# Kernel tuning notes

Hardware: AMD Instinct MI355X
Metric: run time of the kernel (lower is better)

## Reference

```python
import jax, jax.numpy as jnp
import numpy as np

B, T, V, E, H, U = 32, 64, 32000, 300, 512, 512


def setup_inputs() -> dict:
    key = jax.random.key(0)
    ks = jax.random.split(key, 14)
    s = 0.05  # weight scale to keep gates in a sane range
    return {
        "trg_seq": jax.random.randint(ks[0], (B, T), 0, V, dtype=jnp.int32),
        "init_h": jax.random.normal(ks[1], (1, B, U), jnp.float32),
        "init_c": jax.random.normal(ks[2], (1, B, U), jnp.float32),
        "embedding": jax.random.normal(ks[3], (V, E), jnp.float32) * s,
        "Wh": jax.random.normal(ks[4], (H, U), jnp.float32) * s,
        "bh": jax.random.normal(ks[5], (H,), jnp.float32) * s,
        "Wc": jax.random.normal(ks[6], (H, U), jnp.float32) * s,
        "bc": jax.random.normal(ks[7], (H,), jnp.float32) * s,
        "W_ih": jax.random.normal(ks[8], (4 * H, E), jnp.float32) * s,
        "W_hh": jax.random.normal(ks[9], (4 * H, H), jnp.float32) * s,
        "b_ih": jax.random.normal(ks[10], (4 * H,), jnp.float32) * s,
        "b_hh": jax.random.normal(ks[11], (4 * H,), jnp.float32) * s,
        "W_logit": jax.random.normal(ks[12], (V, H), jnp.float32) * s,
        "b_logit": jax.random.normal(ks[13], (V,), jnp.float32) * s,
    }


def reference(trg_seq, init_h, init_c, embedding, Wh, bh, Wc, bc,
              W_ih, W_hh, b_ih, b_hh, W_logit, b_logit):
    # form_init: linear transform of encoder states -> LSTM initial h/c
    h0 = init_h[0] @ Wh.T + bh  # [B, H]
    c0 = init_c[0] @ Wc.T + bc  # [B, H]

    emb = embedding[trg_seq]                       # [B, T, E]
    x_gates = jnp.einsum('bte,ge->btg', emb, W_ih) + b_ih + b_hh  # [B, T, 4H]

    def step(carry, xg_t):
        h, c = carry
        gates = xg_t + h @ W_hh.T                  # [B, 4H]
        i, f, g, o = jnp.split(gates, 4, axis=-1)  # torch gate order i,f,g,o
        i, f, o = jax.nn.sigmoid(i), jax.nn.sigmoid(f), jax.nn.sigmoid(o)
        g = jnp.tanh(g)
        c = f * c + i * g
        h = o * jnp.tanh(c)
        return (h, c), h

    _, hs = jax.lax.scan(step, (h0, c0), x_gates.transpose(1, 0, 2))  # hs: [T, B, H]
    logits = jnp.tanh(hs) @ W_logit.T + b_logit    # [T, B, V]
    return logits.transpose(1, 0, 2)               # [B, T, V]
```

## Files before the change

### kernel.cpp

```cpp
#include <hip/hip_runtime.h>
#include <hip/hip_cooperative_groups.h>

typedef unsigned short u16;
typedef __attribute__((ext_vector_type(8))) unsigned short us8;
typedef __attribute__((ext_vector_type(8))) __bf16 bf16x8;
typedef __attribute__((ext_vector_type(4))) float f32x4;

#define B_ 32
#define T_ 64
#define V_ 32000
#define E_ 300
#define H_ 512
#define G4_ 2048
#define NBLK_ 32
#define NG_   224
#define NT_TILES 250
#define NM_TILES 16

__device__ __forceinline__ u16 f2b(float f){
  unsigned int x = __builtin_bit_cast(unsigned int, f);
  unsigned int r = (x + 0x7FFFu + ((x >> 16) & 1u)) >> 16;
  return (u16)r;
}
__device__ __forceinline__ float sigm(float x){ return 1.0f/(1.0f+expf(-x)); }

__device__ __forceinline__ void gload16(const u16* g, u16* l){
  __builtin_amdgcn_global_load_lds(
      (const __attribute__((address_space(1))) void*)g,
      (__attribute__((address_space(3))) void*)l, 16, 0, 0);
}

__global__ __launch_bounds__(256) void k_init(
    const float* __restrict__ init_h, const float* __restrict__ init_c,
    const float* __restrict__ Wh, const float* __restrict__ bh,
    const float* __restrict__ Wc, const float* __restrict__ bc,
    float* __restrict__ h0out, float* __restrict__ c0out,
    unsigned int* __restrict__ flag)
{
  if (blockIdx.x == 0){ flag[threadIdx.x] = 0u; flag[threadIdx.x + 256] = 0u; }
  int idx = blockIdx.x*blockDim.x + threadIdx.x;
  int sel = idx >> 14;
  int r = idx & 16383;
  int b = r >> 9, j = r & 511;
  const float* x = (sel ? init_c : init_h) + b*H_;
  const float* w = (sel ? Wc : Wh) + (size_t)j*H_;
  const float* bias = sel ? bc : bh;
  float acc = 0.f;
  for (int k = 0; k < H_; k += 8){
    f32x4 x0 = *(const f32x4*)(x + k), x1 = *(const f32x4*)(x + k + 4);
    f32x4 w0 = *(const f32x4*)(w + k), w1 = *(const f32x4*)(w + k + 4);
    acc += x0[0]*w0[0] + x0[1]*w0[1] + x0[2]*w0[2] + x0[3]*w0[3];
    acc += x1[0]*w1[0] + x1[1]*w1[1] + x1[2]*w1[2] + x1[3]*w1[3];
  }
  acc += bias[j];
  (sel ? c0out : h0out)[b*H_ + j] = acc;
}

__global__ __launch_bounds__(256) void k_cvt(
    const float* __restrict__ W, u16* __restrict__ W16)
{
  size_t i = ((size_t)blockIdx.x*256 + threadIdx.x)*8;
  f32x4 a = *(const f32x4*)(W + i);
  f32x4 b = *(const f32x4*)(W + i + 4);
  us8 u;
  u[0]=f2b(a[0]); u[1]=f2b(a[1]); u[2]=f2b(a[2]); u[3]=f2b(a[3]);
  u[4]=f2b(b[0]); u[5]=f2b(b[1]); u[6]=f2b(b[2]); u[7]=f2b(b[3]);
  *(us8*)(W16 + i) = u;
}

__global__ __launch_bounds__(256) void k_xgates(
    const float* __restrict__ emb, const float* __restrict__ Wih,
    const int* __restrict__ trg, const float* __restrict__ bih,
    const float* __restrict__ bhh, float* __restrict__ xg)
{
  __shared__ u16 As[128][40];
  __shared__ u16 Bs[128][40];
  const int bn0 = blockIdx.x*128, bm0 = blockIdx.y*128;
  const int tid = threadIdx.x;
  const int w = tid>>6, lane = tid&63;
  const int wr = w>>1, wc = w&1, lr = lane&15, lk = lane>>4;
  const int srow = tid>>1, half = tid&1;
  const int R = bm0 + srow;
  const int tt = R>>5, bb = R&31;
  const int token = trg[bb*T_ + tt];
  const float* arow = emb + (size_t)token*E_;
  const float* brow = Wih + (size_t)(bn0+srow)*E_;
  f32x4 acc[4][4] = {};
  for (int k0 = 0; k0 < E_; k0 += 32){
    int cbase = k0 + half*16;
    if (k0 + 32 <= E_){
      f32x4 a0=*(const f32x4*)(arow+cbase),    a1=*(const f32x4*)(arow+cbase+4);
      f32x4 a2=*(const f32x4*)(arow+cbase+8),  a3=*(const f32x4*)(arow+cbase+12);
      f32x4 b0=*(const f32x4*)(brow+cbase),    b1=*(const f32x4*)(brow+cbase+4);
      f32x4 b2=*(const f32x4*)(brow+cbase+8),  b3=*(const f32x4*)(brow+cbase+12);
      us8 ua, ub;
      ua[0]=f2b(a0[0]); ua[1]=f2b(a0[1]); ua[2]=f2b(a0[2]); ua[3]=f2b(a0[3]);
      ua[4]=f2b(a1[0]); ua[5]=f2b(a1[1]); ua[6]=f2b(a1[2]); ua[7]=f2b(a1[3]);
      ub[0]=f2b(a2[0]); ub[1]=f2b(a2[1]); ub[2]=f2b(a2[2]); ub[3]=f2b(a2[3]);
      ub[4]=f2b(a3[0]); ub[5]=f2b(a3[1]); ub[6]=f2b(a3[2]); ub[7]=f2b(a3[3]);
      *(us8*)&As[srow][half*16]   = ua;
      *(us8*)&As[srow][half*16+8] = ub;
      us8 va, vb;
      va[0]=f2b(b0[0]); va[1]=f2b(b0[1]); va[2]=f2b(b0[2]); va[3]=f2b(b0[3]);
      va[4]=f2b(b1[0]); va[5]=f2b(b1[1]); va[6]=f2b(b1[2]); va[7]=f2b(b1[3]);
      vb[0]=f2b(b2[0]); vb[1]=f2b(b2[1]); vb[2]=f2b(b2[2]); vb[3]=f2b(b2[3]);
      vb[4]=f2b(b3[0]); vb[5]=f2b(b3[1]); vb[6]=f2b(b3[2]); vb[7]=f2b(b3[3]);
      *(us8*)&Bs[srow][half*16]   = va;
      *(us8*)&Bs[srow][half*16+8] = vb;
    } else {
      for (int i = 0; i < 16; i++){
        int c = cbase + i;
        As[srow][half*16+i] = (c < E_) ? f2b(arow[c]) : (u16)0;
        Bs[srow][half*16+i] = (c < E_) ? f2b(brow[c]) : (u16)0;
      }
    }
    __syncthreads();
    bf16x8 af[4], bfr[4];
    #pragma unroll
    for (int m = 0; m < 4; m++) af[m] = *(const bf16x8*)&As[wr*64 + m*16 + lr][lk*8];
    #pragma unroll
    for (int n = 0; n < 4; n++) bfr[n] = *(const bf16x8*)&Bs[wc*64 + n*16 + lr][lk*8];
    #pragma unroll
    for (int m = 0; m < 4; m++)
      #pragma unroll
      for (int n = 0; n < 4; n++)
        acc[m][n] = __builtin_amdgcn_mfma_f32_16x16x32_bf16(af[m], bfr[n], acc[m][n], 0, 0, 0);
    __syncthreads();
  }
  #pragma unroll
  for (int n = 0; n < 4; n++){
    int col = bn0 + wc*64 + n*16 + lr;
    float bv = bih[col] + bhh[col];
    #pragma unroll
    for (int m = 0; m < 4; m++){
      #pragma unroll
      for (int i = 0; i < 4; i++){
        int row = bm0 + wr*64 + m*16 + lk*4 + i;
        xg[(size_t)row*G4_ + col] = acc[m][n][i] + bv;
      }
    }
  }
}

__global__ __launch_bounds__(512, 4) void k_mega(
    const float* __restrict__ Whh, const float* __restrict__ xg,
    const float* __restrict__ h0, const float* __restrict__ c0,
    u16* __restrict__ h_g, u16* __restrict__ A_buf,
    unsigned int* __restrict__ flag,
    const u16* __restrict__ W16, const float* __restrict__ bias,
    float* __restrict__ out)
{
  __shared__ __align__(16) char smem[41472];
  const int tid = threadIdx.x;

  if (blockIdx.x < NBLK_){
    u16 (*hl)[520] = (u16(*)[520])smem;
    float (*gb)[32][16] = (float(*)[32][16])(smem + 33280);
    const int bj = blockIdx.x;
    const int wv = tid >> 6, lane = tid & 63;
    const int g = wv >> 1, m = wv & 1;
    const int lr = lane & 15, lk = lane >> 4;

    bf16x8 bw[16];
    {
      const float* wsrc = Whh + (size_t)(g*H_ + bj*16 + lr)*H_;
      #pragma unroll
      for (int ks = 0; ks < 16; ks++){
        f32x4 w0 = *(const f32x4*)(wsrc + ks*32 + lk*8);
        f32x4 w1 = *(const f32x4*)(wsrc + ks*32 + lk*8 + 4);
        us8 u;
        u[0]=f2b(w0[0]); u[1]=f2b(w0[1]); u[2]=f2b(w0[2]); u[3]=f2b(w0[3]);
        u[4]=f2b(w1[0]); u[5]=f2b(w1[1]); u[6]=f2b(w1[2]); u[7]=f2b(w1[3]);
        bw[ks] = __builtin_bit_cast(bf16x8, u);
      }
    }
    const int ub = tid >> 4, uj = tid & 15;
    float c_reg = c0[ub*H_ + bj*16 + uj];

    {
      int r = tid >> 4, seg = tid & 15;
      const float* src = h0 + r*H_ + seg*32;
      #pragma unroll
      for (int q = 0; q < 4; q++){
        f32x4 v0 = *(const f32x4*)(src + q*8);
        f32x4 v1 = *(const f32x4*)(src + q*8 + 4);
        us8 u;
        u[0]=f2b(v0[0]); u[1]=f2b(v0[1]); u[2]=f2b(v0[2]); u[3]=f2b(v0[3]);
        u[4]=f2b(v1[0]); u[5]=f2b(v1[1]); u[6]=f2b(v1[2]); u[7]=f2b(v1[3]);
        *(us8*)&hl[r][seg*32 + q*8] = u;
      }
    }
    __syncthreads();

    for (int t = 0; t < T_; t++){
      const float* xr = xg + (size_t)t*(B_*G4_) + ub*G4_ + bj*16 + uj;
      float x0 = xr[0*H_], x1 = xr[1*H_], x2 = xr[2*H_], x3 = xr[3*H_];

      f32x4 acc = {0.f, 0.f, 0.f, 0.f};
      #pragma unroll
      for (int ks = 0; ks < 16; ks++){
        bf16x8 a = *(const bf16x8*)&hl[m*16 + lr][ks*32 + lk*8];
        acc = __builtin_amdgcn_mfma_f32_16x16x32_bf16(a, bw[ks], acc, 0, 0, 0);
      }
      #pragma unroll
      for (int i = 0; i < 4; i++)
        gb[g][m*16 + lk*4 + i][lr] = acc[i];
      __syncthreads();

      float gi = sigm(gb[0][ub][uj] + x0);
      float gf = sigm(gb[1][ub][uj] + x1);
      float gg = tanhf(gb[2][ub][uj] + x2);
      float go = sigm(gb[3][ub][uj] + x3);
      c_reg = gf*c_reg + gi*gg;
      float h = go * tanhf(c_reg);
      int p = (t+1) & 1;
      h_g[p*(B_*H_) + bj*(B_*16) + tid] = f2b(h);

      __syncthreads();
      if (t < T_-1 && tid == 0)
        __hip_atomic_store(&flag[bj*16], (unsigned)(t+1),
                           __ATOMIC_RELEASE, __HIP_MEMORY_SCOPE_AGENT);

      A_buf[(size_t)t*(B_*H_) + ub*H_ + bj*16 + uj] = f2b(tanhf(h));
      if (t == T_-1) break;

      if (tid < 64){
        unsigned want = (unsigned)(t+1), guard = 0;
        while (__hip_atomic_load(&flag[(tid&31)*16], __ATOMIC_ACQUIRE,
                                 __HIP_MEMORY_SCOPE_AGENT) < want
               && guard < (1u<<18)) { __builtin_amdgcn_s_sleep(1); ++guard; }
      }
      __syncthreads();

      {
        int r = tid >> 4, seg = tid & 15;
        const u16* hb = h_g + p*(B_*H_);
        const u16* p0 = hb + (seg*2)  *(B_*16) + r*16;
        const u16* p1 = hb + (seg*2+1)*(B_*16) + r*16;
        us8 v0 = *(const us8*)(p0);
        us8 v1 = *(const us8*)(p0 + 8);
        us8 v2 = *(const us8*)(p1);
        us8 v3 = *(const us8*)(p1 + 8);
        *(us8*)&hl[r][seg*32]      = v0;
        *(us8*)&hl[r][seg*32 + 8]  = v1;
        *(us8*)&hl[r][seg*32 + 16] = v2;
        *(us8*)&hl[r][seg*32 + 24] = v3;
      }
      __syncthreads();
    }
    __syncthreads();
    if (tid == 0)
      __hip_atomic_store(&flag[bj*16], 65u,
                         __ATOMIC_RELEASE, __HIP_MEMORY_SCOPE_AGENT);
  } else {
    u16* As = (u16*)smem;
    u16* Bs = (u16*)(smem + 8192);
    const int w = tid>>6, lane = tid&63;
    const int wr = w & 1, wc = w >> 1;
    const int lr = lane&15, lk = lane>>4;
    const int srow = w*16 + (lane>>2);
    const int cb   = ((lane&3)*16) ^ (((srow>>1)&3)<<4);
    u16* adst = &As[(w*16)*32];
    u16* bdst = &Bs[(w*16)*32];
    const int nt0 = (int)blockIdx.x - NBLK_;

    for (int mt = 0; mt < NM_TILES; mt++){
      const unsigned want = (mt < 15) ? (unsigned)(4*mt + 5) : 65u;
      if (tid < 64){
        unsigned guard = 0;
        for (;;){
          unsigned v = __hip_atomic_load(&flag[(tid&31)*16], __ATOMIC_RELAXED,
                                         __HIP_MEMORY_SCOPE_AGENT);
          if (__all(v >= want) || guard > (1u<<20)) break;
          __builtin_amdgcn_s_sleep(16); ++guard;
        }
        __builtin_amdgcn_fence(__ATOMIC_ACQUIRE, "agent");
      }
      __syncthreads();

      const int bm0 = mt*128;
      for (int nt = nt0; nt < NT_TILES; nt += NG_){
        const int bn0 = nt*128;
        const u16* aptr = A_buf + (size_t)(bm0+srow)*H_ + (cb>>1);
        const u16* bptr = W16   + (size_t)(bn0+srow)*H_ + (cb>>1);
        f32x4 acc[4][2] = {};
        for (int k0 = 0; k0 < H_; k0 += 32){
          gload16(aptr + k0, adst);
          gload16(bptr + k0, bdst);
          __syncthreads();
          bf16x8 af[4], bfr[2];
          #pragma unroll
          for (int m = 0; m < 4; m++){
            int row = wr*64 + m*16 + lr;
            af[m] = *(const bf16x8*)((const char*)As + row*64 + ((lk*16) ^ (((row>>1)&3)<<4)));
          }
          #pragma unroll
          for (int n = 0; n < 2; n++){
            int row = wc*32 + n*16 + lr;
            bfr[n] = *(const bf16x8*)((const char*)Bs + row*64 + ((lk*16) ^ (((row>>1)&3)<<4)));
          }
          #pragma unroll
          for (int m = 0; m < 4; m++)
            #pragma unroll
            for (int n = 0; n < 2; n++)
              acc[m][n] = __builtin_amdgcn_mfma_f32_16x16x32_bf16(af[m], bfr[n], acc[m][n], 0, 0, 0);
          __syncthreads();
        }
        #pragma unroll
        for (int n = 0; n < 2; n++){
          int col = bn0 + wc*32 + n*16 + lr;
          float bv = bias[col];
          #pragma unroll
          for (int m = 0; m < 4; m++){
            #pragma unroll
            for (int i = 0; i < 4; i++){
              int row = bm0 + wr*64 + m*16 + lk*4 + i;
              int t = row>>5, b = row&31;
              __builtin_nontemporal_store(acc[m][n][i] + bv,
                  &out[(size_t)b*((size_t)T_*V_) + (size_t)t*V_ + col]);
            }
          }
        }
      }
    }
  }
}

__global__ __launch_bounds__(512) void k_scan(
    const float* __restrict__ Whh, const float* __restrict__ xg,
    const float* __restrict__ h0, const float* __restrict__ c0,
    u16* __restrict__ h_g, u16* __restrict__ A_buf,
    unsigned int* __restrict__ flag)
{
  __shared__ u16 hl[32][520];
  __shared__ float gb[4][32][16];
  const int bj = blockIdx.x;
  const int tid = threadIdx.x;
  const int wv = tid >> 6, lane = tid & 63;
  const int g = wv >> 1, m = wv & 1;
  const int lr = lane & 15, lk = lane >> 4;
  bf16x8 bw[16];
  {
    const float* wsrc = Whh + (size_t)(g*H_ + bj*16 + lr)*H_;
    #pragma unroll
    for (int ks = 0; ks < 16; ks++){
      f32x4 w0 = *(const f32x4*)(wsrc + ks*32 + lk*8);
      f32x4 w1 = *(const f32x4*)(wsrc + ks*32 + lk*8 + 4);
      us8 u;
      u[0]=f2b(w0[0]); u[1]=f2b(w0[1]); u[2]=f2b(w0[2]); u[3]=f2b(w0[3]);
      u[4]=f2b(w1[0]); u[5]=f2b(w1[1]); u[6]=f2b(w1[2]); u[7]=f2b(w1[3]);
      bw[ks] = __builtin_bit_cast(bf16x8, u);
    }
  }
  const int ub = tid >> 4, uj = tid & 15;
  float c_reg = c0[ub*H_ + bj*16 + uj];
  {
    int r = tid >> 4, seg = tid & 15;
    const float* src = h0 + r*H_ + seg*32;
    #pragma unroll
    for (int q = 0; q < 4; q++){
      f32x4 v0 = *(const f32x4*)(src + q*8);
      f32x4 v1 = *(const f32x4*)(src + q*8 + 4);
      us8 u;
      u[0]=f2b(v0[0]); u[1]=f2b(v0[1]); u[2]=f2b(v0[2]); u[3]=f2b(v0[3]);
      u[4]=f2b(v1[0]); u[5]=f2b(v1[1]); u[6]=f2b(v1[2]); u[7]=f2b(v1[3]);
      *(us8*)&hl[r][seg*32 + q*8] = u;
    }
  }
  __syncthreads();
  for (int t = 0; t < T_; t++){
    const float* xr = xg + (size_t)t*(B_*G4_) + ub*G4_ + bj*16 + uj;
    float x0 = xr[0*H_], x1 = xr[1*H_], x2 = xr[2*H_], x3 = xr[3*H_];
    f32x4 acc = {0.f, 0.f, 0.f, 0.f};
    #pragma unroll
    for (int ks = 0; ks < 16; ks++){
      bf16x8 a = *(const bf16x8*)&hl[m*16 + lr][ks*32 + lk*8];
      acc = __builtin_amdgcn_mfma_f32_16x16x32_bf16(a, bw[ks], acc, 0, 0, 0);
    }
    #pragma unroll
    for (int i = 0; i < 4; i++)
      gb[g][m*16 + lk*4 + i][lr] = acc[i];
    __syncthreads();
    float gi = sigm(gb[0][ub][uj] + x0);
    float gf = sigm(gb[1][ub][uj] + x1);
    float gg = tanhf(gb[2][ub][uj] + x2);
    float go = sigm(gb[3][ub][uj] + x3);
    c_reg = gf*c_reg + gi*gg;
    float h = go * tanhf(c_reg);
    int p = (t+1) & 1;
    h_g[p*(B_*H_) + bj*(B_*16) + tid] = f2b(h);
    __syncthreads();
    if (t < T_-1 && tid == 0)
      __hip_atomic_store(&flag[bj*16], (unsigned)(t+1),
                         __ATOMIC_RELEASE, __HIP_MEMORY_SCOPE_AGENT);
    A_buf[(size_t)t*(B_*H_) + ub*H_ + bj*16 + uj] = f2b(tanhf(h));
    if (t == T_-1) break;
    if (tid < 64){
      unsigned want = (unsigned)(t+1), guard = 0;
      while (__hip_atomic_load(&flag[(tid&31)*16], __ATOMIC_ACQUIRE,
                               __HIP_MEMORY_SCOPE_AGENT) < want
             && guard < (1u<<18)) { __builtin_amdgcn_s_sleep(1); ++guard; }
    }
    __syncthreads();
    {
      int r = tid >> 4, seg = tid & 15;
      const u16* hb = h_g + p*(B_*H_);
      const u16* p0 = hb + (seg*2)  *(B_*16) + r*16;
      const u16* p1 = hb + (seg*2+1)*(B_*16) + r*16;
      us8 v0 = *(const us8*)(p0);
      us8 v1 = *(const us8*)(p0 + 8);
      us8 v2 = *(const us8*)(p1);
      us8 v3 = *(const us8*)(p1 + 8);
      *(us8*)&hl[r][seg*32]      = v0;
      *(us8*)&hl[r][seg*32 + 8]  = v1;
      *(us8*)&hl[r][seg*32 + 16] = v2;
      *(us8*)&hl[r][seg*32 + 24] = v3;
    }
    __syncthreads();
  }
}

__global__ __launch_bounds__(256) void k_logits16(
    const u16* __restrict__ A, const u16* __restrict__ W16,
    const float* __restrict__ bias, float* __restrict__ out)
{
  __shared__ u16 As[128*32];
  __shared__ u16 Bs[128*32];
  int bid = blockIdx.y*16 + blockIdx.x;
  int nbid = (bid & 7)*500 + (bid >> 3);
  const int bm0 = (nbid & 15)*128;
  const int bn0 = (nbid >> 4)*128;
  const int tid = threadIdx.x;
  const int w = tid>>6, lane = tid&63;
  const int wr = w>>1, wc = w&1, lr = lane&15, lk = lane>>4;
  const int srow = w*32 + (lane>>2);
  const int cb   = ((lane&3)*16) ^ (((srow>>1)&3)<<4);
  const u16* aptr = A   + (size_t)(bm0+srow)*H_ + (cb>>1);
  const u16* bptr = W16 + (size_t)(bn0+srow)*H_ + (cb>>1);
  u16* adst0 = &As[(w*32)*32];
  u16* adst1 = &As[(w*32+16)*32];
  u16* bdst0 = &Bs[(w*32)*32];
  u16* bdst1 = &Bs[(w*32+16)*32];
  f32x4 acc[4][4] = {};
  for (int k0 = 0; k0 < H_; k0 += 32){
    gload16(aptr + k0,          adst0);
    gload16(aptr + k0 + 16*H_,  adst1);
    gload16(bptr + k0,          bdst0);
    gload16(bptr + k0 + 16*H_,  bdst1);
    __syncthreads();
    bf16x8 af[4], bfr[4];
    #pragma unroll
    for (int m = 0; m < 4; m++){
      int row = wr*64 + m*16 + lr;
      af[m] = *(const bf16x8*)((const char*)As + row*64 + ((lk*16) ^ (((row>>1)&3)<<4)));
    }
    #pragma unroll
    for (int n = 0; n < 4; n++){
      int row = wc*64 + n*16 + lr;
      bfr[n] = *(const bf16x8*)((const char*)Bs + row*64 + ((lk*16) ^ (((row>>1)&3)<<4)));
    }
    #pragma unroll
    for (int m = 0; m < 4; m++)
      #pragma unroll
      for (int n = 0; n < 4; n++)
        acc[m][n] = __builtin_amdgcn_mfma_f32_16x16x32_bf16(af[m], bfr[n], acc[m][n], 0, 0, 0);
    __syncthreads();
  }
  #pragma unroll
  for (int n = 0; n < 4; n++){
    int col = bn0 + wc*64 + n*16 + lr;
    float bv = bias[col];
    #pragma unroll
    for (int m = 0; m < 4; m++){
      #pragma unroll
      for (int i = 0; i < 4; i++){
        int row = bm0 + wr*64 + m*16 + lk*4 + i;
        int t = row>>5, b = row&31;
        __builtin_nontemporal_store(acc[m][n][i] + bv,
            &out[(size_t)b*((size_t)T_*V_) + (size_t)t*V_ + col]);
      }
    }
  }
}

__global__ __launch_bounds__(256) void k_logits(
    const u16* __restrict__ A, const float* __restrict__ W,
    const float* __restrict__ bias, float* __restrict__ out)
{
  __shared__ u16 As[128][40];
  __shared__ u16 Bs[128][40];
  const int bm0 = blockIdx.x*128, bn0 = blockIdx.y*128;
  const int tid = threadIdx.x;
  const int w = tid>>6, lane = tid&63;
  const int wr = w>>1, wc = w&1, lr = lane&15, lk = lane>>4;
  const int srow = tid>>1, half = tid&1;
  const u16*   arow = A + (size_t)(bm0+srow)*H_;
  const float* brow = W + (size_t)(bn0+srow)*H_;
  f32x4 acc[4][4] = {};
  for (int k0 = 0; k0 < H_; k0 += 32){
    us8 a0 = *(const us8*)(arow + k0 + half*16);
    us8 a1 = *(const us8*)(arow + k0 + half*16 + 8);
    f32x4 b0 = *(const f32x4*)(brow + k0 + half*16);
    f32x4 b1 = *(const f32x4*)(brow + k0 + half*16 + 4);
    f32x4 b2 = *(const f32x4*)(brow + k0 + half*16 + 8);
    f32x4 b3 = *(const f32x4*)(brow + k0 + half*16 + 12);
    *(us8*)&As[srow][half*16]   = a0;
    *(us8*)&As[srow][half*16+8] = a1;
    us8 vb0, vb1;
    vb0[0]=f2b(b0[0]); vb0[1]=f2b(b0[1]); vb0[2]=f2b(b0[2]); vb0[3]=f2b(b0[3]);
    vb0[4]=f2b(b1[0]); vb0[5]=f2b(b1[1]); vb0[6]=f2b(b1[2]); vb0[7]=f2b(b1[3]);
    vb1[0]=f2b(b2[0]); vb1[1]=f2b(b2[1]); vb1[2]=f2b(b2[2]); vb1[3]=f2b(b2[3]);
    vb1[4]=f2b(b3[0]); vb1[5]=f2b(b3[1]); vb1[6]=f2b(b3[2]); vb1[7]=f2b(b3[3]);
    *(us8*)&Bs[srow][half*16]   = vb0;
    *(us8*)&Bs[srow][half*16+8] = vb1;
    __syncthreads();
    bf16x8 af[4], bfr[4];
    #pragma unroll
    for (int m = 0; m < 4; m++) af[m] = *(const bf16x8*)&As[wr*64 + m*16 + lr][lk*8];
    #pragma unroll
    for (int n = 0; n < 4; n++) bfr[n] = *(const bf16x8*)&Bs[wc*64 + n*16 + lr][lk*8];
    #pragma unroll
    for (int m = 0; m < 4; m++)
      #pragma unroll
      for (int n = 0; n < 4; n++)
        acc[m][n] = __builtin_amdgcn_mfma_f32_16x16x32_bf16(af[m], bfr[n], acc[m][n], 0, 0, 0);
    __syncthreads();
  }
  #pragma unroll
  for (int n = 0; n < 4; n++){
    int col = bn0 + wc*64 + n*16 + lr;
    float bv = bias[col];
    #pragma unroll
    for (int m = 0; m < 4; m++){
      #pragma unroll
      for (int i = 0; i < 4; i++){
        int row = bm0 + wr*64 + m*16 + lk*4 + i;
        int t = row>>5, b = row&31;
        out[(size_t)b*((size_t)T_*V_) + (size_t)t*V_ + col] = acc[m][n][i] + bv;
      }
    }
  }
}

extern "C" void kernel_launch(void* const* d_in, const int* in_sizes, int n_in,
                              void* d_out, int out_size, void* d_ws, size_t ws_size,
                              hipStream_t stream)
{
  const int*   trg    = (const int*)d_in[0];
  const float* init_h = (const float*)d_in[1];
  const float* init_c = (const float*)d_in[2];
  const float* emb    = (const float*)d_in[3];
  const float* Wh     = (const float*)d_in[4];
  const float* bh     = (const float*)d_in[5];
  const float* Wc     = (const float*)d_in[6];
  const float* bc     = (const float*)d_in[7];
  const float* Wih    = (const float*)d_in[8];
  const float* Whh    = (const float*)d_in[9];
  const float* bih    = (const float*)d_in[10];
  const float* bhh    = (const float*)d_in[11];
  const float* Wlogit = (const float*)d_in[12];
  const float* blogit = (const float*)d_in[13];
  float* out = (float*)d_out;

  char* ws = (char*)d_ws;
  float*        xg    = (float*)(ws);
  float*        h0    = (float*)(ws + 16777216);
  float*        c0    = (float*)(ws + 16842752);
  u16*          A_buf = (u16*)  (ws + 16908288);
  u16*          h_g   = (u16*)  (ws + 19005440);
  unsigned int* flag  = (unsigned int*)(ws + 19136512);
  u16*          W16   = (u16*)  (ws + 19138560);
  const size_t need_w16 = 19138560ull + 32768000ull;
  const bool use_w16 = (ws_size >= need_w16);

  hipLaunchKernelGGL(k_init, dim3(128), dim3(256), 0, stream,
                     init_h, init_c, Wh, bh, Wc, bc, h0, c0, flag);
  if (use_w16)
    hipLaunchKernelGGL(k_cvt, dim3((V_*H_)/(256*8)), dim3(256), 0, stream,
                       Wlogit, W16);
  hipLaunchKernelGGL(k_xgates, dim3(16, 16), dim3(256), 0, stream,
                     emb, Wih, trg, bih, bhh, xg);
  if (use_w16){
    void* args[] = { (void*)&Whh, (void*)&xg, (void*)&h0, (void*)&c0,
                     (void*)&h_g, (void*)&A_buf, (void*)&flag,
                     (void*)&W16, (void*)&blogit, (void*)&out };
    hipError_t merr = hipLaunchCooperativeKernel((void*)k_mega,
                          dim3(NBLK_ + NG_), dim3(512), args, 0, stream);
    if (merr != hipSuccess){
      void* sargs[] = { (void*)&Whh, (void*)&xg, (void*)&h0, (void*)&c0,
                        (void*)&h_g, (void*)&A_buf, (void*)&flag };
      hipLaunchCooperativeKernel((void*)k_scan, dim3(NBLK_), dim3(512),
                                 sargs, 0, stream);
      hipLaunchKernelGGL(k_logits16, dim3(16, 250), dim3(256), 0, stream,
                         A_buf, W16, blogit, out);
    }
  } else {
    void* args[] = { (void*)&Whh, (void*)&xg, (void*)&h0, (void*)&c0,
                     (void*)&h_g, (void*)&A_buf, (void*)&flag };
    hipLaunchCooperativeKernel((void*)k_scan, dim3(NBLK_), dim3(512), args, 0, stream);
    hipLaunchKernelGGL(k_logits, dim3(16, 250), dim3(256), 0, stream,
                       A_buf, Wlogit, blogit, out);
  }
}
```

Before: 499.6 us.

## Add single gate block for logits sync and batch M-tiles per W tile

One dedicated block now polls the 32 scan-block flags and publishes a single gate counter at four coarse milestones (every 16 timesteps). The logits worker blocks wait on that one word instead of each polling all 32 flags, so there is far less atomic polling traffic competing with the recurrent scan. Each worker also processes four M-tiles per N-tile, which may improve reuse of the W tile in cache. The cost is coarser overlap: logits start only after 16-step chunks complete, so more GEMM work may be left after the scan ends. There is also one fewer worker block.

```diff
diff --git a/kernel.cpp b/kernel.cpp
--- a/kernel.cpp
+++ b/kernel.cpp
@@ -13,7 +13,7 @@
 #define H_ 512
 #define G4_ 2048
 #define NBLK_ 32
-#define NG_   224
+#define NWRK_ 223
 #define NT_TILES 250
 #define NM_TILES 16
 
@@ -35,9 +35,12 @@
     const float* __restrict__ Wh, const float* __restrict__ bh,
     const float* __restrict__ Wc, const float* __restrict__ bc,
     float* __restrict__ h0out, float* __restrict__ c0out,
-    unsigned int* __restrict__ flag)
-{
-  if (blockIdx.x == 0){ flag[threadIdx.x] = 0u; flag[threadIdx.x + 256] = 0u; }
+    unsigned int* __restrict__ flag, unsigned int* __restrict__ gate)
+{
+  if (blockIdx.x == 0){
+    flag[threadIdx.x] = 0u; flag[threadIdx.x + 256] = 0u;
+    if (threadIdx.x == 0) gate[0] = 0u;
+  }
   int idx = blockIdx.x*blockDim.x + threadIdx.x;
   int sel = idx >> 14;
   int r = idx & 16383;
@@ -146,7 +149,7 @@
     const float* __restrict__ Whh, const float* __restrict__ xg,
     const float* __restrict__ h0, const float* __restrict__ c0,
     u16* __restrict__ h_g, u16* __restrict__ A_buf,
-    unsigned int* __restrict__ flag,
+    unsigned int* __restrict__ flag, unsigned int* __restrict__ gate,
     const u16* __restrict__ W16, const float* __restrict__ bias,
     float* __restrict__ out)
 {
@@ -252,6 +255,22 @@
     if (tid == 0)
       __hip_atomic_store(&flag[bj*16], 65u,
                          __ATOMIC_RELEASE, __HIP_MEMORY_SCOPE_AGENT);
+  } else if (blockIdx.x == NBLK_){
+    if (tid < 64){
+      for (int q = 0; q < 4; q++){
+        unsigned want = (q < 3) ? (unsigned)(16*q + 17) : 65u;
+        unsigned guard = 0;
+        for (;;){
+          unsigned v = __hip_atomic_load(&flag[(tid&31)*16], __ATOMIC_ACQUIRE,
+                                         __HIP_MEMORY_SCOPE_AGENT);
+          if (__all(v >= want) || guard > (1u<<21)) break;
+          __builtin_amdgcn_s_sleep(2); ++guard;
+        }
+        if (tid == 0)
+          __hip_atomic_store(gate, (unsigned)(q+1),
+                             __ATOMIC_RELEASE, __HIP_MEMORY_SCOPE_AGENT);
+      }
+    }
   } else {
     u16* As = (u16*)smem;
     u16* Bs = (u16*)(smem + 8192);
@@ -262,62 +281,59 @@
     const int cb   = ((lane&3)*16) ^ (((srow>>1)&3)<<4);
     u16* adst = &As[(w*16)*32];
     u16* bdst = &Bs[(w*16)*32];
-    const int nt0 = (int)blockIdx.x - NBLK_;
-
-    for (int mt = 0; mt < NM_TILES; mt++){
-      const unsigned want = (mt < 15) ? (unsigned)(4*mt + 5) : 65u;
-      if (tid < 64){
+    const int wid = (int)blockIdx.x - (NBLK_ + 1);
+
+    for (int q = 0; q < 4; q++){
+      if (tid == 0){
         unsigned guard = 0;
-        for (;;){
-          unsigned v = __hip_atomic_load(&flag[(tid&31)*16], __ATOMIC_RELAXED,
-                                         __HIP_MEMORY_SCOPE_AGENT);
-          if (__all(v >= want) || guard > (1u<<20)) break;
-          __builtin_amdgcn_s_sleep(16); ++guard;
-        }
-        __builtin_amdgcn_fence(__ATOMIC_ACQUIRE, "agent");
+        while (__hip_atomic_load(gate, __ATOMIC_ACQUIRE,
+                                 __HIP_MEMORY_SCOPE_AGENT) < (unsigned)(q+1)
+               && guard < (1u<<21)) { __builtin_amdgcn_s_sleep(8); ++guard; }
       }
       __syncthreads();
 
-      const int bm0 = mt*128;
-      for (int nt = nt0; nt < NT_TILES; nt += NG_){
+      for (int nt = wid; nt < NT_TILES; nt += NWRK_){
         const int bn0 = nt*128;
-        const u16* aptr = A_buf + (size_t)(bm0+srow)*H_ + (cb>>1);
-        const u16* bptr = W16   + (size_t)(bn0+srow)*H_ + (cb>>1);
-        f32x4 acc[4][2] = {};
-        for (int k0 = 0; k0 < H_; k0 += 32){
-          gload16(aptr + k0, adst);
-          gload16(bptr + k0, bdst);
-          __syncthreads();
-          bf16x8 af[4], bfr[2];
-          #pragma unroll
-          for (int m = 0; m < 4; m++){
-            int row = wr*64 + m*16 + lr;
-            af[m] = *(const bf16x8*)((const char*)As + row*64 + ((lk*16) ^ (((row>>1)&3)<<4)));
+        const u16* bpt = W16 + (size_t)(bn0+srow)*H_ + (cb>>1);
+        for (int mtl = 0; mtl < 4; mtl++){
+          const int bm0 = (q*4 + mtl)*128;
+          const u16* apt = A_buf + (size_t)(bm0+srow)*H_ + (cb>>1);
+          f32x4 acc[4][2] = {};
+          for (int k0 = 0; k0 < H_; k0 += 32){
+            gload16(apt + k0, adst);
+            gload16(bpt + k0, bdst);
+            __syncthreads();
+            bf16x8 af[4], bfr[2];
+            #pragma unroll
+            for (int m = 0; m < 4; m++){
+              int row = wr*64 + m*16 + lr;
+              af[m] = *(const bf16x8*)((const char*)As + row*64 + ((lk*16) ^ (((row>>1)&3)<<4)));
+            }
+            #pragma unroll
+            for (int n = 0; n < 2; n++){
+              int row = wc*32 + n*16 + lr;
+              bfr[n] = *(const bf16x8*)((const char*)Bs + row*64 + ((lk*16) ^ (((row>>1)&3)<<4)));
+            }
+            #pragma unroll
+            for (int m = 0; m < 4; m++)
+              #pragma unroll
+              for (int n = 0; n < 2; n++)
+                acc[m][n] = __builtin_amdgcn_mfma_f32_16x16x32_bf16(af[m], bfr[n], acc[m][n], 0, 0, 0);
+            __syncthreads();
           }
           #pragma unroll
           for (int n = 0; n < 2; n++){
-            int row = wc*32 + n*16 + lr;
-            bfr[n] = *(const bf16x8*)((const char*)Bs + row*64 + ((lk*16) ^ (((row>>1)&3)<<4)));
-          }
-          #pragma unroll
-          for (int m = 0; m < 4; m++)
+            int col = bn0 + wc*32 + n*16 + lr;
+            float bv = bias[col];
             #pragma unroll
-            for (int n = 0; n < 2; n++)
-              acc[m][n] = __builtin_amdgcn_mfma_f32_16x16x32_bf16(af[m], bfr[n], acc[m][n], 0, 0, 0);
-          __syncthreads();
-        }
-        #pragma unroll
-        for (int n = 0; n < 2; n++){
-          int col = bn0 + wc*32 + n*16 + lr;
-          float bv = bias[col];
-          #pragma unroll
-          for (int m = 0; m < 4; m++){
-            #pragma unroll
-            for (int i = 0; i < 4; i++){
-              int row = bm0 + wr*64 + m*16 + lk*4 + i;
-              int t = row>>5, b = row&31;
-              __builtin_nontemporal_store(acc[m][n][i] + bv,
-                  &out[(size_t)b*((size_t)T_*V_) + (size_t)t*V_ + col]);
+            for (int m = 0; m < 4; m++){
+              #pragma unroll
+              for (int i = 0; i < 4; i++){
+                int row = bm0 + wr*64 + m*16 + lk*4 + i;
+                int t = row>>5, b = row&31;
+                __builtin_nontemporal_store(acc[m][n][i] + bv,
+                    &out[(size_t)b*((size_t)T_*V_) + (size_t)t*V_ + col]);
+              }
             }
           }
         }
@@ -569,12 +585,13 @@
   u16*          A_buf = (u16*)  (ws + 16908288);
   u16*          h_g   = (u16*)  (ws + 19005440);
   unsigned int* flag  = (unsigned int*)(ws + 19136512);
-  u16*          W16   = (u16*)  (ws + 19138560);
-  const size_t need_w16 = 19138560ull + 32768000ull;
+  unsigned int* gate  = (unsigned int*)(ws + 19138560);
+  u16*          W16   = (u16*)  (ws + 19138624);
+  const size_t need_w16 = 19138624ull + 32768000ull;
   const bool use_w16 = (ws_size >= need_w16);
 
   hipLaunchKernelGGL(k_init, dim3(128), dim3(256), 0, stream,
-                     init_h, init_c, Wh, bh, Wc, bc, h0, c0, flag);
+                     init_h, init_c, Wh, bh, Wc, bc, h0, c0, flag, gate);
   if (use_w16)
     hipLaunchKernelGGL(k_cvt, dim3((V_*H_)/(256*8)), dim3(256), 0, stream,
                        Wlogit, W16);
@@ -582,10 +599,10 @@
                      emb, Wih, trg, bih, bhh, xg);
   if (use_w16){
     void* args[] = { (void*)&Whh, (void*)&xg, (void*)&h0, (void*)&c0,
-                     (void*)&h_g, (void*)&A_buf, (void*)&flag,
+                     (void*)&h_g, (void*)&A_buf, (void*)&flag, (void*)&gate,
                      (void*)&W16, (void*)&blogit, (void*)&out };
     hipError_t merr = hipLaunchCooperativeKernel((void*)k_mega,
-                          dim3(NBLK_ + NG_), dim3(512), args, 0, stream);
+                          dim3(256), dim3(512), args, 0, stream);
     if (merr != hipSuccess){
       void* sargs[] = { (void*)&Whh, (void*)&xg, (void*)&h0, (void*)&c0,
                         (void*)&h_g, (void*)&A_buf, (void*)&flag };
```

Measured after the change: 855.5 us. 71.3% more time.
